# Optimization experiments

Hardware: AMD Instinct MI355X
Metric: run time of the kernel (lower is better)

Reference implementation:

```python
import jax, jax.numpy as jnp
import numpy as np

T, B, E, H = 2048, 2, 2048, 16
D = E // H  # 128


def setup_inputs() -> dict:
    key = jax.random.key(0)
    ks = jax.random.split(key, 4)
    query = jax.random.normal(ks[0], (T, B, E), dtype=jnp.float32)
    Wqkv = jax.random.normal(ks[1], (3 * E, E), dtype=jnp.float32) * 0.02
    bqkv = jnp.zeros((3 * E,), dtype=jnp.float32)
    Wo = jax.random.normal(ks[2], (E, E), dtype=jnp.float32) * 0.02
    bo = jnp.zeros((E,), dtype=jnp.float32)
    # Llama rotary frequencies: freqs_cis[t, j] = exp(i * t * theta^{-2j/D})
    inv_freq = 1.0 / (10000.0 ** (np.arange(0, D, 2, dtype=np.float32) / D))  # (D/2,)
    angles = np.arange(T, dtype=np.float32)[:, None] * inv_freq[None, :]       # (T, D/2)
    freqs_cos = jnp.asarray(np.cos(angles), dtype=jnp.float32)
    freqs_sin = jnp.asarray(np.sin(angles), dtype=jnp.float32)
    return {"query": query, "Wqkv": Wqkv, "bqkv": bqkv, "Wo": Wo, "bo": bo,
            "freqs_cos": freqs_cos, "freqs_sin": freqs_sin}


def _apply_rope(x, cos, sin):
    # Faithful to metaseq: x is (T, B, E) but view()-ed as (B, T, H, D);
    # jnp.reshape is the same row-major reinterpretation as torch .view().
    xr = x.reshape(B, T, H, D // 2, 2)
    x0, x1 = xr[..., 0], xr[..., 1]
    c = cos[None, :, None, :]  # broadcast over batch and heads, seq_dim=1
    s = sin[None, :, None, :]
    o0 = x0 * c - x1 * s
    o1 = x0 * s + x1 * c
    return jnp.stack([o0, o1], axis=-1).reshape(T, B, E)


def reference(query, Wqkv, bqkv, Wo, bo, freqs_cos, freqs_sin):
    # Combined QKV projection (ColumnParallelLinear, world_size=1), split order (k, v, q)
    kvq = jnp.einsum('tbe,fe->tbf', query, Wqkv) + bqkv  # (T, B, 3E)
    k, v, q = jnp.split(kvq, 3, axis=-1)
    q = _apply_rope(q, freqs_cos, freqs_sin)
    k = _apply_rope(k, freqs_cos, freqs_sin)
    # scaling split as sqrt(head_dim^-0.5) on both q and k (baddbmm path)
    s = jnp.asarray(D, jnp.float32) ** -0.25
    qb = q.reshape(T, B * H, D).swapaxes(0, 1) * s   # (BH, T, D)
    kb = k.reshape(T, B * H, D).swapaxes(0, 1) * s   # (BH, S, D)
    vb = v.reshape(T, B * H, D).swapaxes(0, 1)       # (BH, S, D)
    scores = jnp.einsum('btd,bsd->bts', qb, kb)      # (BH, T, S)
    causal = jnp.tril(jnp.ones((T, T), dtype=bool))  # ScaledUpperTriangMaskedSoftmax
    scores = jnp.where(causal[None, :, :], scores, jnp.finfo(scores.dtype).min)
    probs = jax.nn.softmax(scores, axis=-1)          # dropout p=0 -> identity
    attn = jnp.einsum('bts,bsd->btd', probs, vb)     # (BH, T, D)
    attn = attn.swapaxes(0, 1).reshape(T, B, E)
    # RowParallelLinear with skip_bias_add=True: bias returned separately (not added)
    out = jnp.einsum('tbe,fe->tbf', attn, Wo)
    return out
```

## Files before the change

kernel.cpp:

```cpp
#include <hip/hip_runtime.h>
#include <stdint.h>

typedef unsigned short u16;
typedef __attribute__((ext_vector_type(4))) float f32x4;
typedef __attribute__((ext_vector_type(8))) short bf16x8;
typedef __attribute__((ext_vector_type(8))) u16 u16x8;

#define T_SEQ  2048
#define EMB    2048
#define HD     128
#define NHEAD  16
#define NTOK   4096
#define NE3    6144
#define SCALE  0.29730177875068026f
#define LOG2E  1.44269504088896f

typedef __attribute__((address_space(3))) char* lds_t;
typedef const __attribute__((address_space(1))) char* gl_t;

__device__ __forceinline__ void gld16(const void* g, void* l) {
  __builtin_amdgcn_global_load_lds((gl_t)g, (lds_t)l, 16, 0, 0);
}

__device__ __forceinline__ u16 f2bf(float f) {
  union { float f; uint32_t u; } c; c.f = f;
  uint32_t r = c.u + 0x7fffu + ((c.u >> 16) & 1u);
  return (u16)(r >> 16);
}

__global__ __launch_bounds__(256) void cvt_bf16(const float* __restrict__ in,
                                                u16* __restrict__ out, int n8) {
  int i = blockIdx.x * 256 + threadIdx.x;
  if (i >= n8) return;
  const float4* p = (const float4*)in + (size_t)i * 2;
  float4 a = p[0], b = p[1];
  u16x8 o;
  o[0]=f2bf(a.x); o[1]=f2bf(a.y); o[2]=f2bf(a.z); o[3]=f2bf(a.w);
  o[4]=f2bf(b.x); o[5]=f2bf(b.y); o[6]=f2bf(b.z); o[7]=f2bf(b.w);
  *((u16x8*)out + i) = o;
}


__device__ __forceinline__ bf16x8 rdfrag(const char* slot, int row, int lq) {
  return *(const bf16x8*)(slot + row*64 + ((lq ^ ((row >> 1) & 3)) << 4));
}
__device__ __forceinline__ void stg512(const char* g, int K2, int kbyte,
                                       char* slot, int j, int tid) {
  int lb = j*8192 + tid*16;
  int row = lb >> 6, c = (lb >> 4) & 3;
  gld16(g + (size_t)row*K2 + kbyte + ((c ^ ((row >> 1) & 3)) << 4), slot + lb);
}

template<int EPI>
__global__ __launch_bounds__(512, 2) void gemm256(
    const u16* __restrict__ A, const u16* __restrict__ Bm, int K, int N,
    const float* __restrict__ cosT, const float* __restrict__ sinT,
    const float* __restrict__ bias,
    u16* __restrict__ Qh, u16* __restrict__ Kh, u16* __restrict__ Vt,
    float* __restrict__ Cout)
{
  __shared__ __align__(16) char lds[131072];
  const int tid = threadIdx.x;
  const int lane = tid & 63, w = tid >> 6;
  const int wm = w >> 2, wn = w & 3;
  const int l15 = lane & 15, lq = lane >> 4;

  const int i = blockIdx.x;
  const int regionId = i >> 4, s = i & 15;
  const int bM = (regionId & 3)*4 + (s >> 2);
  const int bN = (regionId >> 2)*4 + (s & 3);

  const char* Ag = (const char*)(A + (size_t)bM * 256 * K);
  const char* Bg = (const char*)(Bm + (size_t)bN * 256 * K);
  const int K2 = K * 2;
  const int nT = K >> 6;

  stg512(Ag, K2, 0,  lds + 0,     0, tid);  stg512(Ag, K2, 0,  lds + 0,     1, tid);
  stg512(Bg, K2, 0,  lds + 32768, 0, tid);  stg512(Bg, K2, 0,  lds + 32768, 1, tid);
  stg512(Ag, K2, 64, lds + 16384, 0, tid);  stg512(Ag, K2, 64, lds + 16384, 1, tid);
  stg512(Bg, K2, 64, lds + 49152, 0, tid);  stg512(Bg, K2, 64, lds + 49152, 1, tid);

  f32x4 acc[8][4] = {};

  for (int t = 0; t < nT; ++t) {
    const int b = t & 1;
    const char* Ab = lds + b*65536;
    const char* Bb = lds + b*65536 + 32768;
    char* Abn = lds + (b^1)*65536;
    char* Bbn = lds + (b^1)*65536 + 32768;
    const int tn = (t + 1 < nT) ? t + 1 : t;

    #pragma unroll
    for (int ks = 0; ks < 2; ++ks) {
      asm volatile("s_waitcnt vmcnt(4)" ::: "memory");
      __builtin_amdgcn_s_barrier();
      __builtin_amdgcn_sched_barrier(0);

      const char* As = Ab + ks*16384;
      const char* Bs = Bb + ks*16384;
      bf16x8 af[8], bf[4];
      #pragma unroll
      for (int j = 0; j < 8; j++) af[j] = rdfrag(As, wm*128 + j*16 + l15, lq);
      #pragma unroll
      for (int j = 0; j < 4; j++) bf[j] = rdfrag(Bs, wn*64 + j*16 + l15, lq);
      const int kb = tn*128 + ks*64;
      stg512(Ag, K2, kb, Abn + ks*16384, 0, tid);
      stg512(Ag, K2, kb, Abn + ks*16384, 1, tid);
      stg512(Bg, K2, kb, Bbn + ks*16384, 0, tid);
      stg512(Bg, K2, kb, Bbn + ks*16384, 1, tid);
      asm volatile("s_waitcnt lgkmcnt(0)" ::: "memory");
      __builtin_amdgcn_sched_barrier(0);
      __builtin_amdgcn_s_setprio(1);
      #pragma unroll
      for (int mi = 0; mi < 8; mi++)
        #pragma unroll
        for (int ni = 0; ni < 4; ni++)
          acc[mi][ni] = __builtin_amdgcn_mfma_f32_16x16x32_bf16(af[mi], bf[ni], acc[mi][ni], 0, 0, 0);
      __builtin_amdgcn_s_setprio(0);
    }
  }
  asm volatile("s_waitcnt vmcnt(0)" ::: "memory");

  if (EPI == 0) {
    #pragma unroll
    for (int mi = 0; mi < 8; mi++) {
      int row = bM*256 + wm*128 + mi*16 + lq*4;
      #pragma unroll
      for (int ni = 0; ni < 4; ni++) {
        int col = bN*256 + wn*64 + ni*16 + l15;
        #pragma unroll
        for (int rr = 0; rr < 4; rr++)
          Cout[(size_t)(row + rr) * N + col] = acc[mi][ni][rr];
      }
    }
  } else {
    const int cbase = bN*256 + wn*64;
    const int seg  = cbase >> 11;
    const int head = (cbase >> 7) & 15;
    #pragma unroll
    for (int mi = 0; mi < 8; mi++) {
      #pragma unroll
      for (int ni = 0; ni < 4; ni++) {
        int col = cbase + ni*16 + l15;
        int d = col & 127;
        float bi = bias[col];
        f32x4 v = acc[mi][ni];
        #pragma unroll
        for (int rr = 0; rr < 4; rr++) {
          int n = bM*256 + wm*128 + mi*16 + lq*4 + rr;
          float val = v[rr] + bi;
          int t = n >> 1, b = n & 1;
          int bh = b*NHEAD + head;
          if (seg == 1) {
            Vt[((size_t)bh*HD + d)*T_SEQ + t] = f2bf(val);
          } else {
            float par = __shfl_xor(val, 1);
            int fidx = d >> 1;
            float cs = cosT[(n & (T_SEQ-1))*64 + fidx];
            float sn = sinT[(n & (T_SEQ-1))*64 + fidx];
            val = (d & 1) ? (par*sn + val*cs) : (val*cs - par*sn);
            val *= SCALE;
            u16* dst = (seg == 0) ? Kh : Qh;
            dst[((size_t)bh*T_SEQ + t)*HD + d] = f2bf(val);
          }
        }
      }
    }
  }
}

__global__ __launch_bounds__(256, 4) void attn_fwd(
    const u16* __restrict__ Qh, const u16* __restrict__ Kh,
    const u16* __restrict__ Vt, u16* __restrict__ O)
{
  const int i = blockIdx.x;
  const int kk = i >> 8, c = i & 255;
  const int bh = (c >> 5) + kk * 8;
  const int b5 = c & 31;
  const int qb = (kk & 1) ? (31 - b5) : b5;

  const int tid = threadIdx.x, lane = tid & 63, w = tid >> 6;
  const int l15 = lane & 15, lq = lane >> 4;

  __shared__ u16 Ks[64*128];
  __shared__ u16 Vs[128*64];
  __shared__ char Ps[4][2048];

  const int q0 = qb*64 + w*16;
  bf16x8 qf[4];
  #pragma unroll
  for (int dc = 0; dc < 4; dc++)
    qf[dc] = *(const bf16x8*)(Qh + ((size_t)bh*T_SEQ + q0 + l15)*HD + dc*32 + lq*8);

  f32x4 o[8] = {};
  float m[4], l_[4];
  #pragma unroll
  for (int r = 0; r < 4; r++) { m[r] = -1e30f; l_[r] = 0.f; }

  const int nkb = qb + 1;
  for (int kb = 0; kb < nkb; ++kb) {
    #pragma unroll
    for (int j = 0; j < 4; j++) {
      int lb = tid*16 + j*4096;
      int row = lb >> 8, bir = lb & 255;
      int sb = bir ^ ((row & 7) << 4);
      gld16((const char*)Kh + (((size_t)bh*T_SEQ + kb*64 + row) << 8) + sb,
            (char*)Ks + lb);
    }
    #pragma unroll
    for (int j = 0; j < 4; j++) {
      int lb = tid*16 + j*4096;
      int row = lb >> 7, bir = lb & 127;
      int sb = bir ^ ((row & 7) << 4);
      gld16((const char*)Vt + ((size_t)(bh*HD + row)*T_SEQ)*2 + kb*128 + sb,
            (char*)Vs + lb);
    }
    __syncthreads();

    f32x4 sacc[4];
    #pragma unroll
    for (int nf = 0; nf < 4; nf++) {
      f32x4 z = {};
      sacc[nf] = z;
      #pragma unroll
      for (int dc = 0; dc < 4; dc++) {
        int row = nf*16 + l15;
        int bir = (dc*64 + lq*16) ^ ((row & 7) << 4);
        bf16x8 kf = *(const bf16x8*)((const char*)Ks + row*256 + bir);
        sacc[nf] = __builtin_amdgcn_mfma_f32_16x16x32_bf16(qf[dc], kf, sacc[nf], 0, 0, 0);
      }
    }

    if (kb == qb) {
      #pragma unroll
      for (int nf = 0; nf < 4; nf++)
        #pragma unroll
        for (int r = 0; r < 4; r++) {
          int key = kb*64 + nf*16 + l15;
          int qr  = q0 + lq*4 + r;
          if (key > qr) sacc[nf][r] = -1e30f;
        }
    }

    #pragma unroll
    for (int r = 0; r < 4; r++) {
      float mx = fmaxf(fmaxf(sacc[0][r], sacc[1][r]), fmaxf(sacc[2][r], sacc[3][r]));
      mx = fmaxf(mx, __shfl_xor(mx, 1));
      mx = fmaxf(mx, __shfl_xor(mx, 2));
      mx = fmaxf(mx, __shfl_xor(mx, 4));
      mx = fmaxf(mx, __shfl_xor(mx, 8));
      float newm = fmaxf(m[r], mx);
      float scale = exp2f((m[r] - newm) * LOG2E);
      float sum = 0.f;
      #pragma unroll
      for (int nf = 0; nf < 4; nf++) {
        float p = exp2f((sacc[nf][r] - newm) * LOG2E);
        sacc[nf][r] = p;
        sum += p;
      }
      sum += __shfl_xor(sum, 1);
      sum += __shfl_xor(sum, 2);
      sum += __shfl_xor(sum, 4);
      sum += __shfl_xor(sum, 8);
      l_[r] = l_[r] * scale + sum;
      m[r] = newm;
      #pragma unroll
      for (int nf = 0; nf < 8; nf++) o[nf][r] *= scale;
    }

    #pragma unroll
    for (int nf = 0; nf < 4; nf++)
      #pragma unroll
      for (int r = 0; r < 4; r++) {
        int prow = lq*4 + r;
        int pbyte = prow*128 + ((((nf*16 + l15)*2)) ^ ((prow & 7) << 4));
        *(u16*)(Ps[w] + pbyte) = f2bf(sacc[nf][r]);
      }

    #pragma unroll
    for (int kc = 0; kc < 2; kc++) {
      int pb = (kc*64 + lq*16) ^ ((l15 & 7) << 4);
      bf16x8 pf = *(const bf16x8*)(Ps[w] + l15*128 + pb);
      #pragma unroll
      for (int nf = 0; nf < 8; nf++) {
        int row = nf*16 + l15;
        int bir = (kc*64 + lq*16) ^ ((row & 7) << 4);
        bf16x8 vf = *(const bf16x8*)((const char*)Vs + row*128 + bir);
        o[nf] = __builtin_amdgcn_mfma_f32_16x16x32_bf16(pf, vf, o[nf], 0, 0, 0);
      }
    }
    __syncthreads();
  }

  const int b = bh >> 4, h = bh & 15;
  #pragma unroll
  for (int r = 0; r < 4; r++) {
    float inv = 1.0f / l_[r];
    int t = q0 + lq*4 + r;
    size_t base = ((size_t)(t*2 + b))*EMB + h*HD;
    #pragma unroll
    for (int nf = 0; nf < 8; nf++)
      O[base + nf*16 + l15] = f2bf(o[nf][r] * inv);
  }
}

extern "C" void kernel_launch(void* const* d_in, const int* in_sizes, int n_in,
                              void* d_out, int out_size, void* d_ws, size_t ws_size,
                              hipStream_t stream) {
  const float* query = (const float*)d_in[0];
  const float* Wqkv  = (const float*)d_in[1];
  const float* bqkv  = (const float*)d_in[2];
  const float* Wo    = (const float*)d_in[3];
  const float* fcos  = (const float*)d_in[5];
  const float* fsin  = (const float*)d_in[6];
  float* out = (float*)d_out;
  char* ws = (char*)d_ws;

  u16* WQb = (u16*)(ws + 0);
  u16* WOb = (u16*)(ws + 25165824);
  u16* A1  = (u16*)(ws + 33554432);
  u16* QH  = (u16*)(ws + 50331648);
  u16* KH  = (u16*)(ws + 67108864);
  u16* VT  = (u16*)(ws + 83886080);

  cvt_bf16<<<4096, 256, 0, stream>>>(query, A1, 1048576);
  cvt_bf16<<<6144, 256, 0, stream>>>(Wqkv, WQb, 1572864);
  cvt_bf16<<<2048, 256, 0, stream>>>(Wo,   WOb,  524288);

  gemm256<1><<<384, 512, 0, stream>>>(A1, WQb, 2048, NE3,
                                      fcos, fsin, bqkv, QH, KH, VT, nullptr);

  attn_fwd<<<1024, 256, 0, stream>>>(QH, KH, VT, A1);

  gemm256<0><<<128, 512, 0, stream>>>(A1, WOb, 2048, EMB,
                                      nullptr, nullptr, nullptr,
                                      nullptr, nullptr, nullptr, out);
}
```

Measured before the change: 365.3 us.

## Triple-buffer GEMM K-loop, retile GEMMs to 256 blocks, double-buffer attention KV

The GEMM becomes a template over the N tile width and uses a 3-stage LDS ring with K steps of 32 instead of double-buffered steps of 64. It is retiled so the QKV projection uses 256x384 tiles (256 blocks) and the output projection uses 256x128 tiles (256 blocks), matching the CU count. The attention kernel double-buffers its K/V tiles in LDS, prefetching two blocks ahead with explicit vmcnt waits, and drops its occupancy hint from 4 to 2 blocks per SM. The goal is to hide global-load latency and fix wave quantization, at the cost of more LDS, more registers in the 384-wide GEMM, and lower attention occupancy.

```diff
diff --git a/kernel.cpp b/kernel.cpp
--- a/kernel.cpp
+++ b/kernel.cpp
@@ -51,15 +51,20 @@
   gld16(g + (size_t)row*K2 + kbyte + ((c ^ ((row >> 1) & 3)) << 4), slot + lb);
 }
 
-template<int EPI>
-__global__ __launch_bounds__(512, 2) void gemm256(
+template<int EPI, int BNT>
+__global__ __launch_bounds__(512) void gemmT(
     const u16* __restrict__ A, const u16* __restrict__ Bm, int K, int N,
     const float* __restrict__ cosT, const float* __restrict__ sinT,
     const float* __restrict__ bias,
     u16* __restrict__ Qh, u16* __restrict__ Kh, u16* __restrict__ Vt,
     float* __restrict__ Cout)
 {
-  __shared__ __align__(16) char lds[131072];
+  constexpr int BSZ = BNT * 64;
+  constexpr int STRIDE = 16384 + BSZ;
+  constexpr int NI = BNT / 64;
+  constexpr int BL = BNT / 128;
+  __shared__ __align__(16) char lds[3 * STRIDE];
+
   const int tid = threadIdx.x;
   const int lane = tid & 63, w = tid >> 6;
   const int wm = w >> 2, wn = w & 3;
@@ -71,53 +76,52 @@
   const int bN = (regionId >> 2)*4 + (s & 3);
 
   const char* Ag = (const char*)(A + (size_t)bM * 256 * K);
-  const char* Bg = (const char*)(Bm + (size_t)bN * 256 * K);
+  const char* Bg = (const char*)(Bm + (size_t)bN * BNT * K);
   const int K2 = K * 2;
-  const int nT = K >> 6;
-
-  stg512(Ag, K2, 0,  lds + 0,     0, tid);  stg512(Ag, K2, 0,  lds + 0,     1, tid);
-  stg512(Bg, K2, 0,  lds + 32768, 0, tid);  stg512(Bg, K2, 0,  lds + 32768, 1, tid);
-  stg512(Ag, K2, 64, lds + 16384, 0, tid);  stg512(Ag, K2, 64, lds + 16384, 1, tid);
-  stg512(Bg, K2, 64, lds + 49152, 0, tid);  stg512(Bg, K2, 64, lds + 49152, 1, tid);
-
-  f32x4 acc[8][4] = {};
+  const int nT = K >> 5;
+
+  #define STAGE_T(t, bufi) do {                                   \
+    const int kb_ = (t) << 6;                                     \
+    char* base_ = lds + (bufi)*STRIDE;                            \
+    stg512(Ag, K2, kb_, base_, 0, tid);                           \
+    stg512(Ag, K2, kb_, base_, 1, tid);                           \
+    _Pragma("unroll")                                             \
+    for (int j_ = 0; j_ < BL; ++j_)                               \
+      stg512(Bg, K2, kb_, base_ + 16384, j_, tid);                \
+  } while (0)
+
+  STAGE_T(0, 0);
+  STAGE_T(1, 1);
+
+  f32x4 acc[8][NI] = {};
 
   for (int t = 0; t < nT; ++t) {
-    const int b = t & 1;
-    const char* Ab = lds + b*65536;
-    const char* Bb = lds + b*65536 + 32768;
-    char* Abn = lds + (b^1)*65536;
-    char* Bbn = lds + (b^1)*65536 + 32768;
-    const int tn = (t + 1 < nT) ? t + 1 : t;
-
-    #pragma unroll
-    for (int ks = 0; ks < 2; ++ks) {
-      asm volatile("s_waitcnt vmcnt(4)" ::: "memory");
-      __builtin_amdgcn_s_barrier();
-      __builtin_amdgcn_sched_barrier(0);
-
-      const char* As = Ab + ks*16384;
-      const char* Bs = Bb + ks*16384;
-      bf16x8 af[8], bf[4];
-      #pragma unroll
-      for (int j = 0; j < 8; j++) af[j] = rdfrag(As, wm*128 + j*16 + l15, lq);
-      #pragma unroll
-      for (int j = 0; j < 4; j++) bf[j] = rdfrag(Bs, wn*64 + j*16 + l15, lq);
-      const int kb = tn*128 + ks*64;
-      stg512(Ag, K2, kb, Abn + ks*16384, 0, tid);
-      stg512(Ag, K2, kb, Abn + ks*16384, 1, tid);
-      stg512(Bg, K2, kb, Bbn + ks*16384, 0, tid);
-      stg512(Bg, K2, kb, Bbn + ks*16384, 1, tid);
-      asm volatile("s_waitcnt lgkmcnt(0)" ::: "memory");
-      __builtin_amdgcn_sched_barrier(0);
-      __builtin_amdgcn_s_setprio(1);
-      #pragma unroll
-      for (int mi = 0; mi < 8; mi++)
-        #pragma unroll
-        for (int ni = 0; ni < 4; ni++)
-          acc[mi][ni] = __builtin_amdgcn_mfma_f32_16x16x32_bf16(af[mi], bf[ni], acc[mi][ni], 0, 0, 0);
-      __builtin_amdgcn_s_setprio(0);
-    }
+    const int bufi = t % 3;
+    const char* Ab = lds + bufi*STRIDE;
+    const char* Bb = Ab + 16384;
+    const int tn2 = (t + 2 < nT) ? t + 2 : nT - 1;
+    const int bufw = (t + 2) % 3;
+
+    if (BNT == 384) asm volatile("s_waitcnt vmcnt(5)" ::: "memory");
+    else            asm volatile("s_waitcnt vmcnt(3)" ::: "memory");
+    __builtin_amdgcn_s_barrier();
+    __builtin_amdgcn_sched_barrier(0);
+
+    bf16x8 af[8], bf[NI];
+    #pragma unroll
+    for (int j = 0; j < 8; j++)  af[j] = rdfrag(Ab, wm*128 + j*16 + l15, lq);
+    #pragma unroll
+    for (int j = 0; j < NI; j++) bf[j] = rdfrag(Bb, wn*(BNT/4) + j*16 + l15, lq);
+    STAGE_T(tn2, bufw);
+    asm volatile("s_waitcnt lgkmcnt(0)" ::: "memory");
+    __builtin_amdgcn_sched_barrier(0);
+    __builtin_amdgcn_s_setprio(1);
+    #pragma unroll
+    for (int mi = 0; mi < 8; mi++)
+      #pragma unroll
+      for (int ni = 0; ni < NI; ni++)
+        acc[mi][ni] = __builtin_amdgcn_mfma_f32_16x16x32_bf16(af[mi], bf[ni], acc[mi][ni], 0, 0, 0);
+    __builtin_amdgcn_s_setprio(0);
   }
   asm volatile("s_waitcnt vmcnt(0)" ::: "memory");
 
@@ -126,24 +130,23 @@
     for (int mi = 0; mi < 8; mi++) {
       int row = bM*256 + wm*128 + mi*16 + lq*4;
       #pragma unroll
-      for (int ni = 0; ni < 4; ni++) {
-        int col = bN*256 + wn*64 + ni*16 + l15;
+      for (int ni = 0; ni < NI; ni++) {
+        int col = bN*BNT + wn*(BNT/4) + ni*16 + l15;
         #pragma unroll
         for (int rr = 0; rr < 4; rr++)
           Cout[(size_t)(row + rr) * N + col] = acc[mi][ni][rr];
       }
     }
   } else {
-    const int cbase = bN*256 + wn*64;
-    const int seg  = cbase >> 11;
-    const int head = (cbase >> 7) & 15;
     #pragma unroll
     for (int mi = 0; mi < 8; mi++) {
       #pragma unroll
-      for (int ni = 0; ni < 4; ni++) {
-        int col = cbase + ni*16 + l15;
-        int d = col & 127;
-        float bi = bias[col];
+      for (int ni = 0; ni < NI; ni++) {
+        const int col16 = bN*BNT + wn*(BNT/4) + ni*16;
+        const int seg  = col16 >> 11;
+        const int head = (col16 >> 7) & 15;
+        const int d = (col16 & 127) + l15;
+        float bi = bias[col16 + l15];
         f32x4 v = acc[mi][ni];
         #pragma unroll
         for (int rr = 0; rr < 4; rr++) {
@@ -167,9 +170,10 @@
       }
     }
   }
-}
-
-__global__ __launch_bounds__(256, 4) void attn_fwd(
+  #undef STAGE_T
+}
+
+__global__ __launch_bounds__(256, 2) void attn_fwd(
     const u16* __restrict__ Qh, const u16* __restrict__ Kh,
     const u16* __restrict__ Vt, u16* __restrict__ O)
 {
@@ -182,8 +186,8 @@
   const int tid = threadIdx.x, lane = tid & 63, w = tid >> 6;
   const int l15 = lane & 15, lq = lane >> 4;
 
-  __shared__ u16 Ks[64*128];
-  __shared__ u16 Vs[128*64];
+  __shared__ u16 Ks[2][64*128];
+  __shared__ u16 Vs[2][128*64];
   __shared__ char Ps[4][2048];
 
   const int q0 = qb*64 + w*16;
@@ -192,30 +196,42 @@
   for (int dc = 0; dc < 4; dc++)
     qf[dc] = *(const bf16x8*)(Qh + ((size_t)bh*T_SEQ + q0 + l15)*HD + dc*32 + lq*8);
 
+  const int nkb = qb + 1;
+
+  #define STAGE_KV(t, b) do {                                              \
+    _Pragma("unroll")                                                      \
+    for (int j_ = 0; j_ < 4; j_++) {                                       \
+      int lb_ = tid*16 + j_*4096;                                          \
+      int row_ = lb_ >> 8, bir_ = lb_ & 255;                               \
+      int sb_ = bir_ ^ ((row_ & 7) << 4);                                  \
+      gld16((const char*)Kh + (((size_t)bh*T_SEQ + (t)*64 + row_) << 8) + sb_, \
+            (char*)Ks[b] + lb_);                                           \
+    }                                                                      \
+    _Pragma("unroll")                                                      \
+    for (int j_ = 0; j_ < 4; j_++) {                                       \
+      int lb_ = tid*16 + j_*4096;                                          \
+      int row_ = lb_ >> 7, bir_ = lb_ & 127;                               \
+      int sb_ = bir_ ^ ((row_ & 7) << 4);                                  \
+      gld16((const char*)Vt + ((size_t)(bh*HD + row_)*T_SEQ)*2 + (t)*128 + sb_, \
+            (char*)Vs[b] + lb_);                                           \
+    }                                                                      \
+  } while (0)
+
+  STAGE_KV(0, 0);
+  STAGE_KV((1 < nkb ? 1 : nkb - 1), 1);
+
   f32x4 o[8] = {};
   float m[4], l_[4];
   #pragma unroll
   for (int r = 0; r < 4; r++) { m[r] = -1e30f; l_[r] = 0.f; }
 
-  const int nkb = qb + 1;
   for (int kb = 0; kb < nkb; ++kb) {
-    #pragma unroll
-    for (int j = 0; j < 4; j++) {
-      int lb = tid*16 + j*4096;
-      int row = lb >> 8, bir = lb & 255;
-      int sb = bir ^ ((row & 7) << 4);
-      gld16((const char*)Kh + (((size_t)bh*T_SEQ + kb*64 + row) << 8) + sb,
-            (char*)Ks + lb);
-    }
-    #pragma unroll
-    for (int j = 0; j < 4; j++) {
-      int lb = tid*16 + j*4096;
-      int row = lb >> 7, bir = lb & 127;
-      int sb = bir ^ ((row & 7) << 4);
-      gld16((const char*)Vt + ((size_t)(bh*HD + row)*T_SEQ)*2 + kb*128 + sb,
-            (char*)Vs + lb);
-    }
-    __syncthreads();
+    asm volatile("s_waitcnt vmcnt(8)" ::: "memory");
+    __builtin_amdgcn_s_barrier();
+    __builtin_amdgcn_sched_barrier(0);
+
+    const char* Kb = (const char*)Ks[kb & 1];
+    const char* Vb = (const char*)Vs[kb & 1];
 
     f32x4 sacc[4];
     #pragma unroll
@@ -226,7 +242,7 @@
       for (int dc = 0; dc < 4; dc++) {
         int row = nf*16 + l15;
         int bir = (dc*64 + lq*16) ^ ((row & 7) << 4);
-        bf16x8 kf = *(const bf16x8*)((const char*)Ks + row*256 + bir);
+        bf16x8 kf = *(const bf16x8*)(Kb + row*256 + bir);
         sacc[nf] = __builtin_amdgcn_mfma_f32_16x16x32_bf16(qf[dc], kf, sacc[nf], 0, 0, 0);
       }
     }
@@ -285,12 +301,17 @@
       for (int nf = 0; nf < 8; nf++) {
         int row = nf*16 + l15;
         int bir = (kc*64 + lq*16) ^ ((row & 7) << 4);
-        bf16x8 vf = *(const bf16x8*)((const char*)Vs + row*128 + bir);
+        bf16x8 vf = *(const bf16x8*)(Vb + row*128 + bir);
         o[nf] = __builtin_amdgcn_mfma_f32_16x16x32_bf16(pf, vf, o[nf], 0, 0, 0);
       }
     }
-    __syncthreads();
+
+    __builtin_amdgcn_s_barrier();
+    const int tnext = (kb + 2 < nkb) ? kb + 2 : nkb - 1;
+    STAGE_KV(tnext, kb & 1);
   }
+  asm volatile("s_waitcnt vmcnt(0)" ::: "memory");
+  #undef STAGE_KV
 
   const int b = bh >> 4, h = bh & 15;
   #pragma unroll
@@ -327,12 +348,12 @@
   cvt_bf16<<<6144, 256, 0, stream>>>(Wqkv, WQb, 1572864);
   cvt_bf16<<<2048, 256, 0, stream>>>(Wo,   WOb,  524288);
 
-  gemm256<1><<<384, 512, 0, stream>>>(A1, WQb, 2048, NE3,
-                                      fcos, fsin, bqkv, QH, KH, VT, nullptr);
+  gemmT<1, 384><<<256, 512, 0, stream>>>(A1, WQb, 2048, NE3,
+                                         fcos, fsin, bqkv, QH, KH, VT, nullptr);
 
   attn_fwd<<<1024, 256, 0, stream>>>(QH, KH, VT, A1);
 
-  gemm256<0><<<128, 512, 0, stream>>>(A1, WOb, 2048, EMB,
-                                      nullptr, nullptr, nullptr,
-                                      nullptr, nullptr, nullptr, out);
-}
+  gemmT<0, 128><<<256, 512, 0, stream>>>(A1, WOb, 2048, EMB,
+                                         nullptr, nullptr, nullptr,
+                                         nullptr, nullptr, nullptr, out);
+}
```

Result: slower. 415.2 us (+13.7%).
